# Kernel optimization log

Hardware: AMD Instinct MI355X
Metric: run time of the kernel (lower is better)

The kernel has to match this reference:

```python
import jax, jax.numpy as jnp
import numpy as np

D = 1024
LD = 64
NTR = 8192
NT = 8192
DY = 128

def setup_inputs() -> dict:
    key = jax.random.key(0)
    k1, k2, k3, k4 = jax.random.split(key, 4)
    xtr = jax.random.normal(k1, (NTR, D), dtype=jnp.float32)
    ytr = jax.random.normal(k2, (NTR, DY), dtype=jnp.float32)
    xt = jax.random.normal(k3, (NT, D), dtype=jnp.float32)
    A = jax.random.normal(k4, (D, LD), dtype=jnp.float32) / (D ** 0.5)
    return {"xtr": xtr, "ytr": ytr, "xt": xt, "A": A}

def reference(xtr, ytr, xt, A):
    # mean-center both train and test features with the train mean
    mu = jnp.mean(xtr, axis=0, keepdims=True)          # [1, d]
    qtr = (xtr - mu) @ A                                # [Ntr, ld]
    qt = (xt - mu) @ A                                  # [Nt, ld]
    scores = jnp.einsum('nl,ml->nm', qt, qtr)           # [Nt, Ntr]
    E = jax.nn.softmax(scores, axis=1)                  # row-wise softmax over train points
    return E @ ytr                                      # [Nt, dy]
```

## Files before the change

kernel.cpp:

```cpp
#include <hip/hip_runtime.h>
#include <hip/hip_bf16.h>

#define D    1024
#define LD   64
#define NTR  8192
#define NT   8192
#define DY   128

#define SHIFT 40.0f
#define NCHUNK 8
#define CHUNK (NTR / NCHUNK)

typedef __attribute__((ext_vector_type(8))) short bf16x8;
typedef __attribute__((ext_vector_type(8))) _Float16 half8;
typedef __attribute__((ext_vector_type(4))) short short4_;
typedef __attribute__((ext_vector_type(4))) float f4;

static __device__ __forceinline__ short f2bf(float f) {
    __hip_bfloat16 h = __float2bfloat16(f);
    short s; __builtin_memcpy(&s, &h, 2); return s;
}
static __device__ __forceinline__ float bf2f(short s) {
    __hip_bfloat16 h; __builtin_memcpy(&h, &s, 2); return __bfloat162float(h);
}
static __device__ __forceinline__ short f2h(float f) {
    _Float16 h = (_Float16)f;
    short s; __builtin_memcpy(&s, &h, 2); return s;
}
static __device__ __forceinline__ float h2f(short s) {
    _Float16 h; __builtin_memcpy(&h, &s, 2); return (float)h;
}

static __device__ __forceinline__ void gload_lds16(const void* g, void* l) {
    __builtin_amdgcn_global_load_lds(
        (const __attribute__((address_space(1))) unsigned int*)g,
        (__attribute__((address_space(3))) unsigned int*)l,
        16, 0, 0);
}

__global__ __launch_bounds__(256) void proj_prep(const float* __restrict__ xt,
                                                 const float* __restrict__ xtr,
                                                 const float* __restrict__ A,
                                                 const float* __restrict__ ytr,
                                                 short* __restrict__ qt_hi,
                                                 short* __restrict__ qt_lo,
                                                 short* __restrict__ ktr,
                                                 float* __restrict__ muAp,
                                                 short* __restrict__ vtile) {
    __shared__ __align__(16) float smem[4224];

    int tid = threadIdx.x;
    int b = blockIdx.x;

    if (b >= 1024) {
        float* tile = smem;
        int bz = b - 1024;
        int t0 = (bz & 127) * 64;
        int d0 = (bz >> 7) * 64;
        int c = tid & 63;
        int r4 = tid >> 6;
        #pragma unroll
        for (int i = 0; i < 16; ++i) {
            int r = i * 4 + r4;
            tile[r * 66 + c] = ytr[(long)(t0 + r) * DY + d0 + c];
        }
        __syncthreads();
        #pragma unroll
        for (int i = 0; i < 16; ++i) {
            int r = i * 4 + r4;
            int t = t0 + c;
            int dy = d0 + r;
            long idx = (long)(t >> 5) * 4096 + (long)dy * 32
                     + ((((t >> 3) & 3) ^ (dy & 3)) << 3) + (t & 7);
            vtile[idx] = f2bf(tile[c * 66 + r]);
        }
        return;
    }

    float (*xbuf)[2][1024] = (float (*)[2][1024])smem;

    int wave = tid >> 6;
    int lane = tid & 63;
    int quad = lane >> 4;
    int l16 = lane & 15;

    bool is_test = b < (NT / 16);
    int row0 = (is_test ? b : b - NT / 16) * 16;
    const float* x = is_test ? xt : xtr;

    int lr = wave * 4 + (lane >> 4);
    int cg = (lane & 15) ^ (lr & 7);
    const float* xsrc = x + (long)(row0 + lr) * D + cg * 4;

    int col = wave * 16 + l16;
    const float* Acol = A + col;

    f4 acc = (f4){0.f, 0.f, 0.f, 0.f};

    int pr0 = ((quad * 2) ^ (l16 & 7)) * 4;
    int pr1 = (((quad * 2) | 1) ^ (l16 & 7)) * 4;

    gload_lds16(xsrc, &xbuf[0][0][wave * 256]);
    gload_lds16(xsrc + 64, &xbuf[0][1][wave * 256]);
    __syncthreads();

    #pragma unroll 1
    for (int s = 0; s < 8; ++s) {
        int cur = s & 1;
        if (s < 7) {
            const float* nsrc = xsrc + (s + 1) * 128;
            gload_lds16(nsrc, &xbuf[cur ^ 1][0][wave * 256]);
            gload_lds16(nsrc + 64, &xbuf[cur ^ 1][1][wave * 256]);
        }

        #pragma unroll
        for (int s2 = 0; s2 < 2; ++s2) {
            int k0 = s * 128 + s2 * 64;

            bf16x8 bh0, bh1, bl0, bl1;
            #pragma unroll
            for (int j = 0; j < 8; ++j) {
                float a0 = Acol[(long)(k0 + quad * 8 + j) * LD];
                float a1 = Acol[(long)(k0 + 32 + quad * 8 + j) * LD];
                short h0 = f2bf(a0);
                short h1 = f2bf(a1);
                bh0[j] = h0; bl0[j] = f2bf(a0 - bf2f(h0));
                bh1[j] = h1; bl1[j] = f2bf(a1 - bf2f(h1));
            }

            const float* xrow = &xbuf[cur][s2][l16 * 64];
            bf16x8 ah[2], al[2];
            #pragma unroll
            for (int h = 0; h < 2; ++h) {
                f4 v0 = *(const f4*)(xrow + h * 32 + pr0);
                f4 v1 = *(const f4*)(xrow + h * 32 + pr1);
                #pragma unroll
                for (int e = 0; e < 4; ++e) {
                    short hi0 = f2bf(v0[e]);
                    short hi1 = f2bf(v1[e]);
                    ah[h][e]     = hi0;
                    ah[h][e + 4] = hi1;
                    al[h][e]     = f2bf(v0[e] - bf2f(hi0));
                    al[h][e + 4] = f2bf(v1[e] - bf2f(hi1));
                }
            }
            acc = __builtin_amdgcn_mfma_f32_16x16x32_bf16(ah[0], bh0, acc, 0, 0, 0);
            acc = __builtin_amdgcn_mfma_f32_16x16x32_bf16(al[0], bh0, acc, 0, 0, 0);
            acc = __builtin_amdgcn_mfma_f32_16x16x32_bf16(ah[0], bl0, acc, 0, 0, 0);
            acc = __builtin_amdgcn_mfma_f32_16x16x32_bf16(ah[1], bh1, acc, 0, 0, 0);
            acc = __builtin_amdgcn_mfma_f32_16x16x32_bf16(al[1], bh1, acc, 0, 0, 0);
            acc = __builtin_amdgcn_mfma_f32_16x16x32_bf16(ah[1], bl1, acc, 0, 0, 0);
        }
        __syncthreads();
    }

    #pragma unroll
    for (int r = 0; r < 4; ++r) {
        int grow = row0 + quad * 4 + r;
        float qv = acc[r];
        if (is_test) {
            short hi = f2h(qv);
            qt_hi[(long)grow * LD + col] = hi;
            qt_lo[(long)grow * LD + col] = f2h(qv - h2f(hi));
        } else {
            int tl = grow & 31;
            long idx = (long)(grow >> 5) * 2048 + tl * 64
                     + ((((col >> 3) ^ (tl & 7))) << 3) + (col & 7);
            ktr[idx] = f2h(qv);
        }
    }

    if (!is_test) {
        float s = acc[0] + acc[1] + acc[2] + acc[3];
        s += __shfl_xor(s, 16);
        s += __shfl_xor(s, 32);
        if (quad == 0) muAp[(long)(b - NT / 16) * 64 + col] = s;
    }
}

__global__ __launch_bounds__(256) void c_kernel(const short* __restrict__ ktr,
                                                const float* __restrict__ muAp,
                                                float* __restrict__ cc) {
    __shared__ float red[4][64];
    __shared__ __align__(16) float muAs[64];
    int l = threadIdx.x & 63;
    int g = threadIdx.x >> 6;
    float ms = 0.f;
    #pragma unroll 8
    for (int p = g; p < 512; p += 4) ms += muAp[(long)p * 64 + l];
    red[g][l] = ms;
    __syncthreads();
    if (threadIdx.x < 64)
        muAs[l] = (red[0][l] + red[1][l] + red[2][l] + red[3][l]) *
                  (1.0f / (float)NTR);
    __syncthreads();

    int t = blockIdx.x * 256 + threadIdx.x;
    int tl = t & 31;
    long rb = (long)(t >> 5) * 2048 + tl * 64;
    float s = SHIFT;
    #pragma unroll
    for (int c = 0; c < 8; ++c) {
        int pos = (c ^ (tl & 7)) << 3;
        bf16x8 h8 = *(const bf16x8*)&ktr[rb + pos];
        f4 m0 = *(const f4*)&muAs[c * 8];
        f4 m1 = *(const f4*)&muAs[c * 8 + 4];
        #pragma unroll
        for (int j = 0; j < 4; ++j) {
            s += h2f(h8[j]) * m0[j];
            s += h2f(h8[j + 4]) * m1[j];
        }
    }
    cc[t] = s;
}

__global__ __launch_bounds__(256, 3) void flash_kernel(const short* __restrict__ qt_hi,
                                                       const short* __restrict__ qt_lo,
                                                       const short* __restrict__ ksw,
                                                       const short* __restrict__ vtile,
                                                       const float* __restrict__ cc,
                                                       short* __restrict__ Opart,
                                                       float* __restrict__ Lpart) {
    __shared__ __align__(16) short kbh[2][2048];
    __shared__ __align__(16) short vbuf[2][4096];
    __shared__ __align__(16) short ptile[4][1280];

    int tid = threadIdx.x;
    int wave = tid >> 6;
    int lane = tid & 63;
    int quad = lane >> 4;
    int l16 = lane & 15;

    int kc = blockIdx.x & 7;
    int qi = blockIdx.x >> 3;
    int q0w = qi * 128 + wave * 32;
    int tile0 = kc * 32;
    int kc0 = kc * CHUNK;

    int soff = wave * 512 + lane * 8;
    int ldso = wave * 512;

    half8 qh[2][2], ql[2][2];
    #pragma unroll
    for (int rt = 0; rt < 2; ++rt) {
        const short* qrh = qt_hi + (long)(q0w + rt * 16 + l16) * LD + quad * 8;
        const short* qrl = qt_lo + (long)(q0w + rt * 16 + l16) * LD + quad * 8;
        qh[rt][0] = *(const half8*)qrh;
        qh[rt][1] = *(const half8*)(qrh + 32);
        ql[rt][0] = *(const half8*)qrl;
        ql[rt][1] = *(const half8*)(qrl + 32);
    }

    bf16x8 onef;
    #pragma unroll
    for (int i = 0; i < 8; ++i) onef[i] = (short)0x3F80;

    f4 Ov[2][8];
    f4 Lv[2];
    #pragma unroll
    for (int rt = 0; rt < 2; ++rt) {
        Lv[rt] = (f4){0.f, 0.f, 0.f, 0.f};
        #pragma unroll
        for (int jt = 0; jt < 8; ++jt) Ov[rt][jt] = (f4){0.f, 0.f, 0.f, 0.f};
    }

    short* myp = &ptile[wave][0];
    const int p0 = ((quad ^ (l16 & 7)) << 3);
    const int pv = ((quad ^ (l16 & 3)) << 3);

    gload_lds16(ksw + (long)tile0 * 2048 + soff, &kbh[0][ldso]);
    gload_lds16(vtile + (long)tile0 * 4096 + soff, &vbuf[0][ldso]);
    gload_lds16(vtile + (long)tile0 * 4096 + 2048 + soff, &vbuf[0][2048 + ldso]);
    __syncthreads();

    #pragma unroll 1
    for (int it = 0; it < 32; ++it) {
        int cur = it & 1;

        f4 cv[2];
        #pragma unroll
        for (int tt = 0; tt < 2; ++tt)
            cv[tt] = *(const f4*)&cc[kc0 + it * 32 + tt * 16 + quad * 4];

        if (it < 31) {
            int nb = cur ^ 1;
            long tb = (long)(tile0 + it + 1);
            gload_lds16(ksw + tb * 2048 + soff, &kbh[nb][ldso]);
            gload_lds16(vtile + tb * 4096 + soff, &vbuf[nb][ldso]);
            gload_lds16(vtile + tb * 4096 + 2048 + soff, &vbuf[nb][2048 + ldso]);
        }

        half8 kh[2][2];
        #pragma unroll
        for (int tt = 0; tt < 2; ++tt) {
            int rb = (tt * 16 + l16) * 64;
            kh[tt][0] = *(const half8*)&kbh[cur][rb + p0];
            kh[tt][1] = *(const half8*)&kbh[cur][rb + (p0 ^ 32)];
        }

        f4 s[2][2];
        #pragma unroll
        for (int rt = 0; rt < 2; ++rt) {
            #pragma unroll
            for (int tt = 0; tt < 2; ++tt) {
                f4 a = (f4){0.f, 0.f, 0.f, 0.f};
                a = __builtin_amdgcn_mfma_f32_16x16x32_f16(kh[tt][0], qh[rt][0], a, 0, 0, 0);
                a = __builtin_amdgcn_mfma_f32_16x16x32_f16(kh[tt][0], ql[rt][0], a, 0, 0, 0);
                a = __builtin_amdgcn_mfma_f32_16x16x32_f16(kh[tt][1], qh[rt][1], a, 0, 0, 0);
                a = __builtin_amdgcn_mfma_f32_16x16x32_f16(kh[tt][1], ql[rt][1], a, 0, 0, 0);
                s[rt][tt] = a;
            }
        }

        #pragma unroll
        for (int rt = 0; rt < 2; ++rt) {
            #pragma unroll
            for (int tt = 0; tt < 2; ++tt) {
                short4_ p4;
                p4[0] = f2bf(__expf(s[rt][tt][0] - cv[tt][0]));
                p4[1] = f2bf(__expf(s[rt][tt][1] - cv[tt][1]));
                p4[2] = f2bf(__expf(s[rt][tt][2] - cv[tt][2]));
                p4[3] = f2bf(__expf(s[rt][tt][3] - cv[tt][3]));
                *(short4_*)&myp[(rt * 16 + l16) * 40 + tt * 16 + quad * 4] = p4;
            }
        }

        bf16x8 vf[8];
        #pragma unroll
        for (int jt = 0; jt < 8; ++jt)
            vf[jt] = *(const bf16x8*)&vbuf[cur][(jt * 16 + l16) * 32 + pv];
        #pragma unroll
        for (int rt = 0; rt < 2; ++rt) {
            bf16x8 pf = *(const bf16x8*)&myp[(rt * 16 + l16) * 40 + quad * 8];
            #pragma unroll
            for (int jt = 0; jt < 8; ++jt)
                Ov[rt][jt] = __builtin_amdgcn_mfma_f32_16x16x32_bf16(pf, vf[jt], Ov[rt][jt], 0, 0, 0);
            Lv[rt] = __builtin_amdgcn_mfma_f32_16x16x32_bf16(pf, onef, Lv[rt], 0, 0, 0);
        }

        __syncthreads();
    }

    long ob = (long)kc * NT;
    #pragma unroll
    for (int rt = 0; rt < 2; ++rt) {
        #pragma unroll
        for (int jt = 0; jt < 8; ++jt) {
            #pragma unroll
            for (int r = 0; r < 4; ++r)
                Opart[(ob + q0w + rt * 16 + quad * 4 + r) * DY + jt * 16 + l16] =
                    f2bf(Ov[rt][jt][r]);
        }
        if (l16 == 0) {
            #pragma unroll
            for (int r = 0; r < 4; ++r)
                Lpart[ob + q0w + rt * 16 + quad * 4 + r] = Lv[rt][r];
        }
    }
}

__global__ __launch_bounds__(256) void finalize_kernel(const short* __restrict__ Opart,
                                                       const float* __restrict__ Lpart,
                                                       float* __restrict__ out) {
    long i = ((long)blockIdx.x * 256 + threadIdx.x) * 8;
    long row = i >> 7;
    float L = 0.f;
    f4 a = (f4){0.f, 0.f, 0.f, 0.f};
    f4 b = (f4){0.f, 0.f, 0.f, 0.f};
    #pragma unroll
    for (int kc = 0; kc < NCHUNK; ++kc) {
        L += Lpart[(long)kc * NT + row];
        bf16x8 o = *(const bf16x8*)&Opart[(long)kc * NT * DY + i];
        #pragma unroll
        for (int j = 0; j < 4; ++j) {
            a[j] += bf2f(o[j]);
            b[j] += bf2f(o[j + 4]);
        }
    }
    float linv = 1.0f / L;
    a *= linv; b *= linv;
    *(f4*)&out[i] = a;
    *(f4*)&out[i + 4] = b;
}

extern "C" void kernel_launch(void* const* d_in, const int* in_sizes, int n_in,
                              void* d_out, int out_size, void* d_ws, size_t ws_size,
                              hipStream_t stream) {
    const float* xtr = (const float*)d_in[0];
    const float* ytr = (const float*)d_in[1];
    const float* xt  = (const float*)d_in[2];
    const float* A   = (const float*)d_in[3];
    float* out = (float*)d_out;

    char* w = (char*)d_ws;
    float* muAp  = (float*)w; w += (size_t)512 * 64 * 4;
    float* cc    = (float*)w; w += (size_t)NTR * 4;
    float* Lpart = (float*)w; w += (size_t)NCHUNK * NT * 4;
    short* Opart = (short*)w; w += (size_t)NCHUNK * NT * DY * 2;
    short* qt_hi  = (short*)w; w += (size_t)NT * LD * 2;
    short* qt_lo  = (short*)w; w += (size_t)NT * LD * 2;
    short* ksw    = (short*)w; w += (size_t)NTR * LD * 2;
    short* vtile  = (short*)w; w += (size_t)DY * NTR * 2;
    (void)ws_size; (void)in_sizes; (void)n_in; (void)out_size;

    proj_prep<<<1280, 256, 0, stream>>>(xt, xtr, A, ytr,
                                        qt_hi, qt_lo, ksw, muAp, vtile);
    c_kernel<<<32, 256, 0, stream>>>(ksw, muAp, cc);
    flash_kernel<<<512, 256, 0, stream>>>(qt_hi, qt_lo, ksw, vtile, cc,
                                          Opart, Lpart);
    finalize_kernel<<<(NT * DY) / (256 * 8), 256, 0, stream>>>(Opart, Lpart, out);
}
```

Measured before the change: 167.4 us.

## Restructure projection per-wave with triple-buffered DMA and split flash into 16 chunks

The projection kernel now has each wave compute a full 16x64 output tile from its own rows, using a private triple-buffered LDS pipeline gated by vmcnt waits instead of block barriers; the grid shrinks accordingly. The flash attention kernel splits the train dimension into 16 chunks instead of 8, doubling its block count to better fill the GPU. This adds more partial outputs for finalize to reduce and more A loads per wave in the projection.

New measurement: 173.8 us. +3.9%, slower.

```diff
diff --git a/kernel.cpp b/kernel.cpp
--- a/kernel.cpp
+++ b/kernel.cpp
@@ -8,7 +8,7 @@
 #define DY   128
 
 #define SHIFT 40.0f
-#define NCHUNK 8
+#define NCHUNK 16
 #define CHUNK (NTR / NCHUNK)
 
 typedef __attribute__((ext_vector_type(8))) short bf16x8;
@@ -37,6 +37,8 @@
         (__attribute__((address_space(3))) unsigned int*)l,
         16, 0, 0);
 }
+
+#define WAIT_VM8() __builtin_amdgcn_s_waitcnt(0x3F78)
 
 __global__ __launch_bounds__(256) void proj_prep(const float* __restrict__ xt,
                                                  const float* __restrict__ xtr,
@@ -47,14 +49,14 @@
                                                  short* __restrict__ ktr,
                                                  float* __restrict__ muAp,
                                                  short* __restrict__ vtile) {
-    __shared__ __align__(16) float smem[4224];
+    __shared__ __align__(16) float xbuf[4][3][1024];
 
     int tid = threadIdx.x;
     int b = blockIdx.x;
 
-    if (b >= 1024) {
-        float* tile = smem;
-        int bz = b - 1024;
+    if (b >= 256) {
+        __shared__ float tile[64][66];
+        int bz = b - 256;
         int t0 = (bz & 127) * 64;
         int d0 = (bz >> 7) * 64;
         int c = tid & 63;
@@ -62,7 +64,7 @@
         #pragma unroll
         for (int i = 0; i < 16; ++i) {
             int r = i * 4 + r4;
-            tile[r * 66 + c] = ytr[(long)(t0 + r) * DY + d0 + c];
+            tile[r][c] = ytr[(long)(t0 + r) * DY + d0 + c];
         }
         __syncthreads();
         #pragma unroll
@@ -72,51 +74,73 @@
             int dy = d0 + r;
             long idx = (long)(t >> 5) * 4096 + (long)dy * 32
                      + ((((t >> 3) & 3) ^ (dy & 3)) << 3) + (t & 7);
-            vtile[idx] = f2bf(tile[c * 66 + r]);
+            vtile[idx] = f2bf(tile[c][r]);
         }
         return;
     }
-
-    float (*xbuf)[2][1024] = (float (*)[2][1024])smem;
 
     int wave = tid >> 6;
     int lane = tid & 63;
     int quad = lane >> 4;
     int l16 = lane & 15;
 
-    bool is_test = b < (NT / 16);
-    int row0 = (is_test ? b : b - NT / 16) * 16;
+    int g = b * 4 + wave;
+    bool is_test = g < (NT / 16);
+    int row0 = (is_test ? g : g - NT / 16) * 16;
     const float* x = is_test ? xt : xtr;
 
-    int lr = wave * 4 + (lane >> 4);
-    int cg = (lane & 15) ^ (lr & 7);
-    const float* xsrc = x + (long)(row0 + lr) * D + cg * 4;
-
-    int col = wave * 16 + l16;
-    const float* Acol = A + col;
-
-    f4 acc = (f4){0.f, 0.f, 0.f, 0.f};
+    int sr = lane >> 4;
+    int cg0 = (lane & 15);
+
+    f4 acc[4];
+    #pragma unroll
+    for (int ct = 0; ct < 4; ++ct) acc[ct] = (f4){0.f, 0.f, 0.f, 0.f};
 
     int pr0 = ((quad * 2) ^ (l16 & 7)) * 4;
     int pr1 = (((quad * 2) | 1) ^ (l16 & 7)) * 4;
 
-    gload_lds16(xsrc, &xbuf[0][0][wave * 256]);
-    gload_lds16(xsrc + 64, &xbuf[0][1][wave * 256]);
-    __syncthreads();
+#define PROJ_DMA(S, BUF)                                                        \
+    {                                                                           \
+        int kk0 = ((S) & 15) * 64;                                              \
+        _Pragma("unroll")                                                       \
+        for (int j = 0; j < 4; ++j) {                                           \
+            int r = j * 4 + sr;                                                 \
+            int cgl = cg0 ^ (r & 7);                                            \
+            gload_lds16(x + (long)(row0 + r) * D + kk0 + cgl * 4,               \
+                        &xbuf[wave][BUF][j * 256]);                             \
+        }                                                                       \
+    }
+
+    PROJ_DMA(0, 0)
+    PROJ_DMA(1, 1)
 
     #pragma unroll 1
-    for (int s = 0; s < 8; ++s) {
-        int cur = s & 1;
-        if (s < 7) {
-            const float* nsrc = xsrc + (s + 1) * 128;
-            gload_lds16(nsrc, &xbuf[cur ^ 1][0][wave * 256]);
-            gload_lds16(nsrc + 64, &xbuf[cur ^ 1][1][wave * 256]);
-        }
-
-        #pragma unroll
-        for (int s2 = 0; s2 < 2; ++s2) {
-            int k0 = s * 128 + s2 * 64;
-
+    for (int s = 0; s < 16; ++s) {
+        int cur = s % 3;
+        PROJ_DMA(s + 2, (s + 2) % 3)
+        WAIT_VM8();
+
+        const float* xrow = &xbuf[wave][cur][l16 * 64];
+        bf16x8 ah[2], al[2];
+        #pragma unroll
+        for (int h = 0; h < 2; ++h) {
+            f4 v0 = *(const f4*)(xrow + h * 32 + pr0);
+            f4 v1 = *(const f4*)(xrow + h * 32 + pr1);
+            #pragma unroll
+            for (int e = 0; e < 4; ++e) {
+                short hi0 = f2bf(v0[e]);
+                short hi1 = f2bf(v1[e]);
+                ah[h][e]     = hi0;
+                ah[h][e + 4] = hi1;
+                al[h][e]     = f2bf(v0[e] - bf2f(hi0));
+                al[h][e + 4] = f2bf(v1[e] - bf2f(hi1));
+            }
+        }
+
+        int k0 = s * 64;
+        #pragma unroll
+        for (int ct = 0; ct < 4; ++ct) {
+            const float* Acol = A + ct * 16 + l16;
             bf16x8 bh0, bh1, bl0, bl1;
             #pragma unroll
             for (int j = 0; j < 8; ++j) {
@@ -127,54 +151,42 @@
                 bh0[j] = h0; bl0[j] = f2bf(a0 - bf2f(h0));
                 bh1[j] = h1; bl1[j] = f2bf(a1 - bf2f(h1));
             }
-
-            const float* xrow = &xbuf[cur][s2][l16 * 64];
-            bf16x8 ah[2], al[2];
-            #pragma unroll
-            for (int h = 0; h < 2; ++h) {
-                f4 v0 = *(const f4*)(xrow + h * 32 + pr0);
-                f4 v1 = *(const f4*)(xrow + h * 32 + pr1);
-                #pragma unroll
-                for (int e = 0; e < 4; ++e) {
-                    short hi0 = f2bf(v0[e]);
-                    short hi1 = f2bf(v1[e]);
-                    ah[h][e]     = hi0;
-                    ah[h][e + 4] = hi1;
-                    al[h][e]     = f2bf(v0[e] - bf2f(hi0));
-                    al[h][e + 4] = f2bf(v1[e] - bf2f(hi1));
-                }
+            f4 a = acc[ct];
+            a = __builtin_amdgcn_mfma_f32_16x16x32_bf16(ah[0], bh0, a, 0, 0, 0);
+            a = __builtin_amdgcn_mfma_f32_16x16x32_bf16(al[0], bh0, a, 0, 0, 0);
+            a = __builtin_amdgcn_mfma_f32_16x16x32_bf16(ah[0], bl0, a, 0, 0, 0);
+            a = __builtin_amdgcn_mfma_f32_16x16x32_bf16(ah[1], bh1, a, 0, 0, 0);
+            a = __builtin_amdgcn_mfma_f32_16x16x32_bf16(al[1], bh1, a, 0, 0, 0);
+            a = __builtin_amdgcn_mfma_f32_16x16x32_bf16(ah[1], bl1, a, 0, 0, 0);
+            acc[ct] = a;
+        }
+    }
+#undef PROJ_DMA
+
+    #pragma unroll
+    for (int ct = 0; ct < 4; ++ct) {
+        int col = ct * 16 + l16;
+        #pragma unroll
+        for (int r = 0; r < 4; ++r) {
+            int grow = row0 + quad * 4 + r;
+            float qv = acc[ct][r];
+            if (is_test) {
+                short hi = f2h(qv);
+                qt_hi[(long)grow * LD + col] = hi;
+                qt_lo[(long)grow * LD + col] = f2h(qv - h2f(hi));
+            } else {
+                int tl = grow & 31;
+                long idx = (long)(grow >> 5) * 2048 + tl * 64
+                         + ((((col >> 3) ^ (tl & 7))) << 3) + (col & 7);
+                ktr[idx] = f2h(qv);
             }
-            acc = __builtin_amdgcn_mfma_f32_16x16x32_bf16(ah[0], bh0, acc, 0, 0, 0);
-            acc = __builtin_amdgcn_mfma_f32_16x16x32_bf16(al[0], bh0, acc, 0, 0, 0);
-            acc = __builtin_amdgcn_mfma_f32_16x16x32_bf16(ah[0], bl0, acc, 0, 0, 0);
-            acc = __builtin_amdgcn_mfma_f32_16x16x32_bf16(ah[1], bh1, acc, 0, 0, 0);
-            acc = __builtin_amdgcn_mfma_f32_16x16x32_bf16(al[1], bh1, acc, 0, 0, 0);
-            acc = __builtin_amdgcn_mfma_f32_16x16x32_bf16(ah[1], bl1, acc, 0, 0, 0);
-        }
-        __syncthreads();
-    }
-
-    #pragma unroll
-    for (int r = 0; r < 4; ++r) {
-        int grow = row0 + quad * 4 + r;
-        float qv = acc[r];
-        if (is_test) {
-            short hi = f2h(qv);
-            qt_hi[(long)grow * LD + col] = hi;
-            qt_lo[(long)grow * LD + col] = f2h(qv - h2f(hi));
-        } else {
-            int tl = grow & 31;
-            long idx = (long)(grow >> 5) * 2048 + tl * 64
-                     + ((((col >> 3) ^ (tl & 7))) << 3) + (col & 7);
-            ktr[idx] = f2h(qv);
-        }
-    }
-
-    if (!is_test) {
-        float s = acc[0] + acc[1] + acc[2] + acc[3];
-        s += __shfl_xor(s, 16);
-        s += __shfl_xor(s, 32);
-        if (quad == 0) muAp[(long)(b - NT / 16) * 64 + col] = s;
+        }
+        if (!is_test) {
+            float s = acc[ct][0] + acc[ct][1] + acc[ct][2] + acc[ct][3];
+            s += __shfl_xor(s, 16);
+            s += __shfl_xor(s, 32);
+            if (quad == 0) muAp[(long)(g - NT / 16) * 64 + col] = s;
+        }
     }
 }
 
@@ -231,10 +243,10 @@
     int quad = lane >> 4;
     int l16 = lane & 15;
 
-    int kc = blockIdx.x & 7;
-    int qi = blockIdx.x >> 3;
+    int kc = blockIdx.x & 15;
+    int qi = blockIdx.x >> 4;
     int q0w = qi * 128 + wave * 32;
-    int tile0 = kc * 32;
+    int tile0 = kc * 16;
     int kc0 = kc * CHUNK;
 
     int soff = wave * 512 + lane * 8;
@@ -274,7 +286,7 @@
     __syncthreads();
 
     #pragma unroll 1
-    for (int it = 0; it < 32; ++it) {
+    for (int it = 0; it < 16; ++it) {
         int cur = it & 1;
 
         f4 cv[2];
@@ -282,7 +294,7 @@
         for (int tt = 0; tt < 2; ++tt)
             cv[tt] = *(const f4*)&cc[kc0 + it * 32 + tt * 16 + quad * 4];
 
-        if (it < 31) {
+        if (it < 15) {
             int nb = cur ^ 1;
             long tb = (long)(tile0 + it + 1);
             gload_lds16(ksw + tb * 2048 + soff, &kbh[nb][ldso]);
@@ -403,10 +415,10 @@
     short* vtile  = (short*)w; w += (size_t)DY * NTR * 2;
     (void)ws_size; (void)in_sizes; (void)n_in; (void)out_size;
 
-    proj_prep<<<1280, 256, 0, stream>>>(xt, xtr, A, ytr,
-                                        qt_hi, qt_lo, ksw, muAp, vtile);
+    proj_prep<<<512, 256, 0, stream>>>(xt, xtr, A, ytr,
+                                       qt_hi, qt_lo, ksw, muAp, vtile);
     c_kernel<<<32, 256, 0, stream>>>(ksw, muAp, cc);
-    flash_kernel<<<512, 256, 0, stream>>>(qt_hi, qt_lo, ksw, vtile, cc,
-                                          Opart, Lpart);
+    flash_kernel<<<1024, 256, 0, stream>>>(qt_hi, qt_lo, ksw, vtile, cc,
+                                           Opart, Lpart);
     finalize_kernel<<<(NT * DY) / (256 * 8), 256, 0, stream>>>(Opart, Lpart, out);
 }
```
